# Performance work log

Hardware: AMD Instinct MI355X
Metric: run time of the kernel (lower is better)

The kernel has to match this reference:

```python
import jax, jax.numpy as jnp
import numpy as np

# --- constants matching DILConfig ---
N_DIFF = 1000      # num_diffusion_steps
STEPS = 4          # inference_steps
S_MAX = 4          # max_scales
BUDGET = 0.2       # entropy_budget
G0 = 2.0           # guidance_strength
ENT_LO = 0.1       # stability_threshold_low
ENT_HI = 0.5       # stability_threshold_high
B, L, C, H = 16, 1024, 128, 512


def setup_inputs() -> dict:
    key = jax.random.key(0)
    ks = jax.random.split(key, 6)
    y_obs = jax.random.normal(ks[0], (B, L, C), dtype=jnp.float32)
    mask = (jax.random.uniform(ks[1], (B, L, C)) > 0.5).astype(jnp.float32)
    z_init = jax.random.normal(ks[2], (B, L, C), dtype=jnp.float32)
    W1 = jax.random.normal(ks[3], (C, H), dtype=jnp.float32) / np.sqrt(C)
    b1 = jnp.zeros((H,), dtype=jnp.float32)
    W2 = jax.random.normal(ks[4], (H, C), dtype=jnp.float32) / np.sqrt(H)
    b2 = jnp.zeros((C,), dtype=jnp.float32)
    tw = jax.random.normal(ks[5], (H,), dtype=jnp.float32)
    return {"y_obs": y_obs, "mask": mask, "z_init": z_init,
            "W1": W1, "b1": b1, "W2": W2, "b2": b2, "tw": tw}


def _dil_forward(y_obs, mask, z_init, W1, b1, W2, b2, tw):
    # diffusion schedule (linear betas)
    betas = jnp.linspace(1e-4, 0.02, N_DIFF, dtype=jnp.float32)
    ac = jnp.cumprod(1.0 - betas)
    alpha = jnp.sqrt(ac)                     # sqrt_alphas_cumprod
    sigma = jnp.sqrt(1.0 - ac)               # sqrt_one_minus_alphas_cumprod
    lam = jnp.log(alpha) - jnp.log(sigma)    # log-SNR/2

    step = N_DIFF // STEPS
    ks = [N_DIFF - 1 - i * step for i in range(STEPS)]

    def score(z, k):
        # epsilon predictor: channel MLP with scalar time feature
        t_feat = jnp.float32(k) / N_DIFF
        h = jax.nn.gelu(jnp.einsum('blc,ch->blh', z, W1) + b1 + t_feat * tw)
        return jnp.einsum('blh,hc->blc', h, W2) + b2

    z = z_init
    for k in ks:  # fixed small unrolled loop over inference steps
        kp = max(k - step, 0)
        eps = score(z, k)                                   # [B,L,C]
        h_lam = lam[kp] - lam[k]
        base_a = alpha[kp] / alpha[k]
        base_b = sigma[kp] * (jnp.exp(h_lam) - 1.0)

        # entropy map: batch-mean |eps| per pixel
        ent_pix = jnp.mean(jnp.abs(eps), axis=0)            # [L,C]

        # self-guidance on observed entries
        obs_err = (z - y_obs) * mask
        guidance = -obs_err / (jnp.var(obs_err) + 1e-8)     # [B,L,C]

        z_new = z
        # coarse -> fine so finer-scale selected nodes overwrite coarser ones
        for s in range(S_MAX - 1, -1, -1):
            w = 2 ** s
            pooled = ent_pix.reshape(L // w, w, C // w, w).mean(axis=(1, 3))
            Knodes = max(1, int(BUDGET * pooled.size))
            _, idx = jax.lax.top_k(pooled.ravel(), Knodes)
            selg = jnp.zeros((pooled.size,), jnp.float32).at[idx].set(1.0)
            selg = selg.reshape(pooled.shape)
            sel = jnp.repeat(jnp.repeat(selg, w, axis=0), w, axis=1)     # [L,C]
            ent_up = jnp.repeat(jnp.repeat(pooled, w, axis=0), w, axis=1)

            # adaptive solver order from entropy stability thresholds
            order = (1.0 + (ent_up > ENT_LO).astype(jnp.float32)
                         + (ent_up > ENT_HI).astype(jnp.float32))
            corr = (1.0 + (order - 1.0) * 0.5 * h_lam
                        + (order - 1.0) * (order - 2.0) / 6.0 * h_lam ** 2)
            gs = G0 * ent_up / (ent_up + 1.0)               # adaptive guidance

            cand = base_a * z - base_b * (corr * eps) + gs * guidance
            z_new = jnp.where(sel[None, :, :] > 0, cand, z_new)
        z = z_new
    return z


def reference(y_obs, mask, z_init, W1, b1, W2, b2, tw):
    return _dil_forward(y_obs, mask, z_init, W1, b1, W2, b2, tw)
```

## Files before the change

kernel.cpp:

```cpp
#include <hip/hip_runtime.h>
#include <math.h>
#include <stdint.h>

#define L_DIM 1024
#define C_DIM 128
#define H_DIM 512
#define B_DIM 16
#define LC (L_DIM * C_DIM)
#define BLC (B_DIM * LC)

typedef __attribute__((ext_vector_type(8))) short short8;
typedef __attribute__((ext_vector_type(4))) float floatx4;

__device__ __forceinline__ unsigned fordbits(unsigned u) {
    return (u & 0x80000000u) ? ~u : (u | 0x80000000u);
}

__device__ __forceinline__ void split3(float x, unsigned& uh, unsigned& um,
                                       unsigned& ul) {
    uh = __float_as_uint(x);
    const float r1 = x - __uint_as_float(uh & 0xffff0000u);
    um = __float_as_uint(r1);
    const float r2 = r1 - __uint_as_float(um & 0xffff0000u);
    ul = __float_as_uint(r2);
}

__device__ __forceinline__ float gelu_fast(float x) {
    const float g = 0.7978845608028654f * (x + 0.044715f * x * x * x);
    const float e = __expf(2.0f * g);
    const float t = 1.0f - 2.0f / (e + 1.0f);
    return 0.5f * x * (1.0f + t);
}

__global__ __launch_bounds__(256) void wsplit_kernel(
    const float* __restrict__ W1, const float* __restrict__ W2,
    unsigned short* __restrict__ W1h, unsigned short* __restrict__ W1m,
    unsigned short* __restrict__ W1l, unsigned short* __restrict__ W2h,
    unsigned short* __restrict__ W2m, unsigned short* __restrict__ W2l,
    unsigned* __restrict__ zeroblk) {
    const int t = blockIdx.x * 256 + threadIdx.x;
    if (t < 16396) zeroblk[t] = 0u;
    unsigned uh, um, ul;
    if (t < 65536) {
        const int j = t & 7, lane = (t >> 3) & 63, nt = (t >> 9) & 31,
                  kt = (t >> 14) & 3;
        const int k = kt * 32 + (lane >> 4) * 8 + j;
        const int n = nt * 16 + (lane & 15);
        split3(W1[k * 512 + n], uh, um, ul);
        W1h[t] = (unsigned short)(uh >> 16);
        W1m[t] = (unsigned short)(um >> 16);
        W1l[t] = (unsigned short)(ul >> 16);
    } else {
        const int t2 = t - 65536;
        const int j = t2 & 7, lane = (t2 >> 3) & 63, nt = (t2 >> 9) & 7,
                  kt = (t2 >> 12) & 15;
        const int k = kt * 32 + (lane >> 4) * 8 + j;
        const int n = nt * 16 + (lane & 15);
        split3(W2[k * 128 + n], uh, um, ul);
        W2h[t2] = (unsigned short)(uh >> 16);
        W2m[t2] = (unsigned short)(um >> 16);
        W2l[t2] = (unsigned short)(ul >> 16);
    }
}

#define MFMA6(AH, AM, AL, BH, BM, BL, ACC)                                    \
    ACC = __builtin_amdgcn_mfma_f32_16x16x32_bf16(AL, BH, ACC, 0, 0, 0);      \
    ACC = __builtin_amdgcn_mfma_f32_16x16x32_bf16(AM, BM, ACC, 0, 0, 0);      \
    ACC = __builtin_amdgcn_mfma_f32_16x16x32_bf16(AH, BL, ACC, 0, 0, 0);      \
    ACC = __builtin_amdgcn_mfma_f32_16x16x32_bf16(AM, BH, ACC, 0, 0, 0);      \
    ACC = __builtin_amdgcn_mfma_f32_16x16x32_bf16(AH, BM, ACC, 0, 0, 0);      \
    ACC = __builtin_amdgcn_mfma_f32_16x16x32_bf16(AH, BH, ACC, 0, 0, 0);

__device__ __forceinline__ int swz(int row, int col) {
    return row * 128 + ((((col >> 3) ^ (row & 15))) << 3) + (col & 7);
}

template <int UPD>
__global__ __launch_bounds__(512, 2) void mlp_kernel(
    float* __restrict__ z, const float* __restrict__ zr,
    const float* __restrict__ y, const float* __restrict__ mk,
    const unsigned short* __restrict__ W1h, const unsigned short* __restrict__ W1m,
    const unsigned short* __restrict__ W1l, const unsigned short* __restrict__ W2h,
    const unsigned short* __restrict__ W2m, const unsigned short* __restrict__ W2l,
    const float* __restrict__ b1, const float* __restrict__ tw,
    const float* __restrict__ b2, float t_feat,
    float* __restrict__ eps_buf, float* __restrict__ ent,
    const float* __restrict__ cA, const float* __restrict__ cB,
    const float* __restrict__ cG, float* __restrict__ accum,
    float* __restrict__ p1, float* __restrict__ p2,
    unsigned* __restrict__ ghist) {
    __shared__ unsigned short zA[3][8192];
    __shared__ unsigned short hA[3][8192];
    __shared__ float entbuf[4][128];
    __shared__ float red1[8], red2[8];
    const int tid = threadIdx.x;
    const int w = tid >> 6, lane = tid & 63;
    const int quad = lane >> 4, m16 = lane & 15;
    const int l0 = blockIdx.x * 4;

    float s1 = 0.f, s2 = 0.f;
#pragma unroll
    for (int e = 0; e < 4; ++e) {
        const int f = (e * 512 + tid) * 4;
        const int r_ = f >> 7, cb = f & 127;
        const int b = r_ & 15, il = r_ >> 4, l = l0 + il;
        const size_t g = ((size_t)b * 1024 + l) * 128 + cb;
        float4 zv = *(const float4*)(zr + g);
        const float4 yv = *(const float4*)(y + g);
        const float4 mv = *(const float4*)(mk + g);
        if (UPD) {
            const float4 ev = *(const float4*)(eps_buf + g);
            const int pix = l * 128 + cb;
            const float4 a4 = *(const float4*)(cA + pix);
            const float4 b4 = *(const float4*)(cB + pix);
            const float4 g4 = *(const float4*)(cG + pix);
            zv.x = a4.x * zv.x - b4.x * ev.x - g4.x * ((zv.x - yv.x) * mv.x);
            zv.y = a4.y * zv.y - b4.y * ev.y - g4.y * ((zv.y - yv.y) * mv.y);
            zv.z = a4.z * zv.z - b4.z * ev.z - g4.z * ((zv.z - yv.z) * mv.z);
            zv.w = a4.w * zv.w - b4.w * ev.w - g4.w * ((zv.w - yv.w) * mv.w);
            *(float4*)(z + g) = zv;
        }
        float oe;
        oe = (zv.x - yv.x) * mv.x; s1 += oe; s2 += oe * oe;
        oe = (zv.y - yv.y) * mv.y; s1 += oe; s2 += oe * oe;
        oe = (zv.z - yv.z) * mv.z; s1 += oe; s2 += oe * oe;
        oe = (zv.w - yv.w) * mv.w; s1 += oe; s2 += oe * oe;

        const int base = swz(r_, cb);
        const float xs[4] = {zv.x, zv.y, zv.z, zv.w};
        ushort4 vh, vm, vl;
        unsigned uh, um, ul;
        split3(xs[0], uh, um, ul); vh.x = uh >> 16; vm.x = um >> 16; vl.x = ul >> 16;
        split3(xs[1], uh, um, ul); vh.y = uh >> 16; vm.y = um >> 16; vl.y = ul >> 16;
        split3(xs[2], uh, um, ul); vh.z = uh >> 16; vm.z = um >> 16; vl.z = ul >> 16;
        split3(xs[3], uh, um, ul); vh.w = uh >> 16; vm.w = um >> 16; vl.w = ul >> 16;
        *(ushort4*)(&zA[0][base]) = vh;
        *(ushort4*)(&zA[1][base]) = vm;
        *(ushort4*)(&zA[2][base]) = vl;
    }
#pragma unroll
    for (int off = 32; off; off >>= 1) {
        s1 += __shfl_down(s1, off);
        s2 += __shfl_down(s2, off);
    }
    if (lane == 0) { red1[w] = s1; red2[w] = s2; }
    __syncthreads();
    if (tid == 0) {
        float a1 = 0.f, a2 = 0.f;
#pragma unroll
        for (int i = 0; i < 8; ++i) { a1 += red1[i]; a2 += red2[i]; }
        atomicAdd(&accum[0], a1);
        atomicAdd(&accum[1], a2);
    }

    floatx4 acc1[16];
#pragma unroll
    for (int i = 0; i < 16; ++i) acc1[i] = (floatx4){0.f, 0.f, 0.f, 0.f};

    {
        short8 Ah[4], Am[4], Al[4];
        short8 bh, bm, bl;
        {
            const size_t off0 = ((size_t)w * 64 + lane) * 8;
            bh = *(const short8*)(W1h + off0);
            bm = *(const short8*)(W1m + off0);
            bl = *(const short8*)(W1l + off0);
        }
#pragma unroll
        for (int it = 0; it < 16; ++it) {
            const int kt = it >> 2, q = it & 3;
            if (q == 0) {
#pragma unroll
                for (int il = 0; il < 4; ++il) {
                    const int fb = swz(il * 16 + m16, kt * 32 + quad * 8);
                    Ah[il] = *(const short8*)(&zA[0][fb]);
                    Am[il] = *(const short8*)(&zA[1][fb]);
                    Al[il] = *(const short8*)(&zA[2][fb]);
                }
            }
            short8 nbh = bh, nbm = bm, nbl = bl;
            if (it < 15) {
                const int itn = it + 1;
                const size_t off =
                    ((size_t)((itn >> 2) * 32 + (itn & 3) * 8 + w) * 64 + lane) * 8;
                nbh = *(const short8*)(W1h + off);
                nbm = *(const short8*)(W1m + off);
                nbl = *(const short8*)(W1l + off);
            }
#pragma unroll
            for (int il = 0; il < 4; ++il) {
                floatx4 a = acc1[q * 4 + il];
                MFMA6(Ah[il], Am[il], Al[il], bh, bm, bl, a);
                acc1[q * 4 + il] = a;
            }
            bh = nbh; bm = nbm; bl = nbl;
        }
    }

    floatx4 acc2[4];
#pragma unroll
    for (int i = 0; i < 4; ++i) acc2[i] = (floatx4){0.f, 0.f, 0.f, 0.f};

    short8 ch, cm, cl;
    {
        const size_t off0 = ((size_t)w * 64 + lane) * 8;
        ch = *(const short8*)(W2h + off0);
        cm = *(const short8*)(W2m + off0);
        cl = *(const short8*)(W2l + off0);
    }
#pragma unroll
    for (int q = 0; q < 4; ++q) {
        {
            const int colg = q * 128 + w * 16 + m16;
            const float bb = b1[colg] + t_feat * tw[colg];
            const int kcol = w * 16 + m16;
#pragma unroll
            for (int il = 0; il < 4; ++il) {
#pragma unroll
                for (int r = 0; r < 4; ++r) {
                    const float x = gelu_fast(acc1[q * 4 + il][r] + bb);
                    unsigned uh, um, ul;
                    split3(x, uh, um, ul);
                    const int idx = swz(il * 16 + quad * 4 + r, kcol);
                    hA[0][idx] = (unsigned short)(uh >> 16);
                    hA[1][idx] = (unsigned short)(um >> 16);
                    hA[2][idx] = (unsigned short)(ul >> 16);
                }
            }
        }
        __syncthreads();

#pragma unroll
        for (int ktl = 0; ktl < 4; ++ktl) {
            const int jt = q * 4 + ktl;
            short8 nch = ch, ncm = cm, ncl = cl;
            if (jt < 15) {
                const size_t off = ((size_t)((jt + 1) * 8 + w) * 64 + lane) * 8;
                nch = *(const short8*)(W2h + off);
                ncm = *(const short8*)(W2m + off);
                ncl = *(const short8*)(W2l + off);
            }
            short8 Ah2[4], Am2[4], Al2[4];
#pragma unroll
            for (int il = 0; il < 4; ++il) {
                const int fb = swz(il * 16 + m16, ktl * 32 + quad * 8);
                Ah2[il] = *(const short8*)(&hA[0][fb]);
                Am2[il] = *(const short8*)(&hA[1][fb]);
                Al2[il] = *(const short8*)(&hA[2][fb]);
            }
#pragma unroll
            for (int il = 0; il < 4; ++il) {
                floatx4 a = acc2[il];
                MFMA6(Ah2[il], Am2[il], Al2[il], ch, cm, cl, a);
                acc2[il] = a;
            }
            ch = nch; cm = ncm; cl = ncl;
        }
        __syncthreads();
    }

    {
        const int col = w * 16 + m16;
        const float bb2 = b2[col];
#pragma unroll
        for (int il = 0; il < 4; ++il) {
            float pa = 0.f;
#pragma unroll
            for (int r = 0; r < 4; ++r) {
                const float e = acc2[il][r] + bb2;
                const int b = quad * 4 + r;
                eps_buf[((size_t)b * 1024 + l0 + il) * 128 + col] = e;
                pa += fabsf(e);
            }
            pa += __shfl_xor(pa, 16);
            pa += __shfl_xor(pa, 32);
            if (quad == 0) {
                const float ev = pa * (1.0f / 16.0f);
                ent[(l0 + il) * 128 + col] = ev;
                entbuf[il][col] = ev;
            }
        }
    }

    unsigned* lhist = (unsigned*)&hA[0][0];
    for (int i = tid; i < 8192; i += 512) lhist[i] = 0u;
    __syncthreads();
    if (tid < 512) {
        const float v = entbuf[tid >> 7][tid & 127];
        const unsigned b = fordbits(__float_as_uint(v)) >> 18;
        atomicAdd(&lhist[b >> 1], 1u << ((b & 1) << 4));
    }
    if (tid < 128) {
        const int ir = tid >> 6, c = tid & 63;
        float s = entbuf[2 * ir][2 * c];
        s += entbuf[2 * ir][2 * c + 1];
        s += entbuf[2 * ir + 1][2 * c];
        s += entbuf[2 * ir + 1][2 * c + 1];
        p1[(2 * (int)blockIdx.x + ir) * 64 + c] = s * 0.25f;
    }
    if (tid < 32) {
        const int c = tid;
        float s = 0.f;
#pragma unroll
        for (int ii = 0; ii < 4; ++ii) {
            s += entbuf[ii][4 * c];
            s += entbuf[ii][4 * c + 1];
            s += entbuf[ii][4 * c + 2];
            s += entbuf[ii][4 * c + 3];
        }
        p2[(int)blockIdx.x * 32 + c] = s * 0.0625f;
    }
    __syncthreads();
    for (int i = tid; i < 8192; i += 512) {
        const unsigned v = lhist[i];
        if (v & 0xFFFFu) atomicAdd(&ghist[2 * i], v & 0xFFFFu);
        if (v >> 16) atomicAdd(&ghist[2 * i + 1], v >> 16);
    }
}


#define CAND_CAP 16384

template <int NPT4, int N, unsigned K>
__device__ __forceinline__ void small_select_vals(
    const float4* xv, unsigned* __restrict__ gout, const int t,
    const int w8, unsigned* __restrict__ histcand,
    unsigned* __restrict__ part, unsigned (*hrep)[512],
    unsigned* sh_b, unsigned* sh_krem, unsigned* sh_cnt, unsigned* sh_d,
    unsigned* sh_k2) {
    unsigned u[NPT4 * 4];
#pragma unroll
    for (int i = 0; i < NPT4; ++i) {
        u[4 * i + 0] = fordbits(__float_as_uint(xv[i].x));
        u[4 * i + 1] = fordbits(__float_as_uint(xv[i].y));
        u[4 * i + 2] = fordbits(__float_as_uint(xv[i].z));
        u[4 * i + 3] = fordbits(__float_as_uint(xv[i].w));
    }
    if (t == 0) { *sh_b = 0u; *sh_krem = 1u; *sh_cnt = 0u; *sh_d = 0u; *sh_k2 = 1u; }
    for (int i = t; i < 16384; i += 1024) histcand[i] = 0u;
    __syncthreads();
#pragma unroll
    for (int j = 0; j < NPT4 * 4; ++j) atomicAdd(&histcand[u[j] >> 18], 1u);
    __syncthreads();
    {
        unsigned s = 0;
#pragma unroll
        for (int j = 0; j < 16; ++j) s += histcand[t * 16 + j];
        part[t] = s;
    }
    __syncthreads();
    for (int off = 1; off < 1024; off <<= 1) {
        const unsigned v = (t + off < 1024) ? part[t + off] : 0u;
        __syncthreads();
        part[t] += v;
        __syncthreads();
    }
    {
        const unsigned suf = part[t];
        const unsigned sufn = (t < 1023) ? part[t + 1] : 0u;
        if (suf >= K && sufn < K) {
            unsigned run = sufn;
            for (int b = 15; b >= 0; --b) {
                const unsigned hb = histcand[t * 16 + b];
                run += hb;
                if (run >= K) {
                    *sh_b = (unsigned)(t * 16 + b);
                    *sh_krem = K - (run - hb);
                    break;
                }
            }
        }
    }
    __syncthreads();
    const unsigned b14 = *sh_b;
    unsigned krem = *sh_krem;
    __syncthreads();
#pragma unroll
    for (int j = 0; j < NPT4 * 4; ++j)
        if ((u[j] >> 18) == b14) {
            const unsigned p = atomicAdd(sh_cnt, 1u);
            if (p < CAND_CAP) histcand[p] = u[j];
        }
    __syncthreads();
    const unsigned cnt = *sh_cnt;
    const bool inlds = (cnt <= CAND_CAP);
    for (int i = t; i < 4096; i += 1024) ((unsigned*)hrep)[i] = 0u;
    __syncthreads();
    if (inlds) {
        for (unsigned i = t; i < cnt; i += 1024)
            atomicAdd(&hrep[w8][(histcand[i] >> 9) & 511u], 1u);
    } else {
#pragma unroll
        for (int j = 0; j < NPT4 * 4; ++j)
            if ((u[j] >> 18) == b14)
                atomicAdd(&hrep[w8][(u[j] >> 9) & 511u], 1u);
    }
    __syncthreads();
    if (t < 512) {
        unsigned s = 0;
#pragma unroll
        for (int r = 0; r < 8; ++r) s += hrep[r][t];
        part[t] = s;
    }
    __syncthreads();
    for (int off = 1; off < 512; off <<= 1) {
        unsigned v = 0u;
        if (t < 512) v = (t + off < 512) ? part[t + off] : 0u;
        __syncthreads();
        if (t < 512) part[t] += v;
        __syncthreads();
    }
    if (t < 512) {
        const unsigned suf = part[t];
        const unsigned sufn = (t < 511) ? part[t + 1] : 0u;
        if (suf >= krem && sufn < krem) { *sh_d = (unsigned)t; *sh_k2 = krem - sufn; }
    }
    __syncthreads();
    const unsigned dA = *sh_d;
    krem = *sh_k2;
    __syncthreads();
    for (int i = t; i < 4096; i += 1024) ((unsigned*)hrep)[i] = 0u;
    __syncthreads();
    if (inlds) {
        for (unsigned i = t; i < cnt; i += 1024) {
            const unsigned c = histcand[i];
            if (((c >> 9) & 511u) == dA) atomicAdd(&hrep[w8][c & 511u], 1u);
        }
    } else {
#pragma unroll
        for (int j = 0; j < NPT4 * 4; ++j)
            if ((u[j] >> 18) == b14 && ((u[j] >> 9) & 511u) == dA)
                atomicAdd(&hrep[w8][u[j] & 511u], 1u);
    }
    __syncthreads();
    if (t < 512) {
        unsigned s = 0;
#pragma unroll
        for (int r = 0; r < 8; ++r) s += hrep[r][t];
        part[t] = s;
    }
    __syncthreads();
    for (int off = 1; off < 512; off <<= 1) {
        unsigned v = 0u;
        if (t < 512) v = (t + off < 512) ? part[t + off] : 0u;
        __syncthreads();
        if (t < 512) part[t] += v;
        __syncthreads();
    }
    if (t < 512) {
        const unsigned suf = part[t];
        const unsigned sufn = (t < 511) ? part[t + 1] : 0u;
        if (suf >= krem && sufn < krem)
            gout[0] = (b14 << 18) | (dA << 9) | (unsigned)t;
    }
}

__global__ __launch_bounds__(1024, 1) void thresh_kernel(
    const float* __restrict__ ent, const float* __restrict__ p1,
    const float* __restrict__ p2, float* __restrict__ p3,
    const unsigned* __restrict__ ghist, unsigned* __restrict__ gprefix) {
    const int scale = blockIdx.x, t = threadIdx.x;
    __shared__ unsigned histcand[16384];
    __shared__ unsigned part[1024];
    __shared__ unsigned hrep[8][512];
    __shared__ unsigned sh_b, sh_krem, sh_cnt, sh_d, sh_k2;
    const int w8 = (t >> 6) & 7;

    if (scale == 1) {
        float4 xv[8];
#pragma unroll
        for (int i = 0; i < 8; ++i) xv[i] = ((const float4*)p1)[t + i * 1024];
        small_select_vals<8, 32768, 6553u>(xv, &gprefix[1], t, w8, histcand,
                                           part, hrep, &sh_b, &sh_krem,
                                           &sh_cnt, &sh_d, &sh_k2);
        return;
    }
    if (scale == 2) {
        float4 xv[2];
#pragma unroll
        for (int i = 0; i < 2; ++i) xv[i] = ((const float4*)p2)[t + i * 1024];
        small_select_vals<2, 8192, 1638u>(xv, &gprefix[2], t, w8, histcand,
                                          part, hrep, &sh_b, &sh_krem,
                                          &sh_cnt, &sh_d, &sh_k2);
        return;
    }
    if (scale == 3) {
        float4 xv[1];
        if (t < 512) {
            float sv[4];
#pragma unroll
            for (int jdx = 0; jdx < 4; ++jdx) {
                const int e = t * 4 + jdx;
                const int r = e >> 4, c = e & 15;
                float s = 0.f;
#pragma unroll
                for (int ii = 0; ii < 8; ++ii) {
                    const float4 ea =
                        *(const float4*)(ent + (((r * 8 + ii) << 7) + c * 8));
                    const float4 eb =
                        *(const float4*)(ent + (((r * 8 + ii) << 7) + c * 8 + 4));
                    s += ea.x; s += ea.y; s += ea.z; s += ea.w;
                    s += eb.x; s += eb.y; s += eb.z; s += eb.w;
                }
                sv[jdx] = s * (1.0f / 64.0f);
            }
            xv[0] = (float4){sv[0], sv[1], sv[2], sv[3]};
            *(float4*)(p3 + t * 4) = xv[0];
        } else {
            xv[0] = (float4){-1e30f, -1e30f, -1e30f, -1e30f};
        }
        small_select_vals<1, 2048, 409u>(xv, &gprefix[3], t, w8, histcand,
                                         part, hrep, &sh_b, &sh_krem,
                                         &sh_cnt, &sh_d, &sh_k2);
        return;
    }

    const unsigned K = 26214u;
    if (t == 0) { sh_b = 0u; sh_krem = 1u; sh_cnt = 0u; sh_d = 0u; sh_k2 = 1u; }

    {
        unsigned s = 0;
        const uint4* h4 = (const uint4*)(ghist + t * 16);
#pragma unroll
        for (int j = 0; j < 4; ++j) {
            const uint4 x = h4[j];
            s += x.x + x.y + x.z + x.w;
        }
        part[t] = s;
    }
    __syncthreads();
    for (int off = 1; off < 1024; off <<= 1) {
        const unsigned v = (t + off < 1024) ? part[t + off] : 0u;
        __syncthreads();
        part[t] += v;
        __syncthreads();
    }
    {
        const unsigned suf = part[t];
        const unsigned sufn = (t < 1023) ? part[t + 1] : 0u;
        if (suf >= K && sufn < K) {
            unsigned run = sufn;
            for (int b = 15; b >= 0; --b) {
                const unsigned hb = ghist[t * 16 + b];
                run += hb;
                if (run >= K) {
                    sh_b = (unsigned)(t * 16 + b);
                    sh_krem = K - (run - hb);
                    break;
                }
            }
        }
    }
    __syncthreads();
    const unsigned b14 = sh_b;
    unsigned krem = sh_krem;

    for (int base = 0; base < 32768; base += 8192) {
        float4 w4[8];
#pragma unroll
        for (int i = 0; i < 8; ++i)
            w4[i] = ((const float4*)ent)[base + i * 1024 + t];
#pragma unroll
        for (int i = 0; i < 8; ++i) {
            const float xs[4] = {w4[i].x, w4[i].y, w4[i].z, w4[i].w};
#pragma unroll
            for (int j = 0; j < 4; ++j) {
                const unsigned uu = fordbits(__float_as_uint(xs[j]));
                if ((uu >> 18) == b14) {
                    const unsigned p = atomicAdd(&sh_cnt, 1u);
                    if (p < CAND_CAP) histcand[p] = uu;
                }
            }
        }
    }
    __syncthreads();
    const unsigned cnt = sh_cnt;
    const bool inlds = (cnt <= CAND_CAP);

    for (int i = t; i < 4096; i += 1024) ((unsigned*)hrep)[i] = 0u;
    __syncthreads();
    if (inlds) {
        for (unsigned i = t; i < cnt; i += 1024)
            atomicAdd(&hrep[w8][(histcand[i] >> 9) & 511u], 1u);
    } else {
        for (int base = 0; base < 32768; base += 8192) {
            float4 w4[8];
#pragma unroll
            for (int i = 0; i < 8; ++i)
                w4[i] = ((const float4*)ent)[base + i * 1024 + t];
#pragma unroll
            for (int i = 0; i < 8; ++i) {
                const float xs[4] = {w4[i].x, w4[i].y, w4[i].z, w4[i].w};
#pragma unroll
                for (int j = 0; j < 4; ++j) {
                    const unsigned uu = fordbits(__float_as_uint(xs[j]));
                    if ((uu >> 18) == b14)
                        atomicAdd(&hrep[w8][(uu >> 9) & 511u], 1u);
                }
            }
        }
    }
    __syncthreads();
    if (t < 512) {
        unsigned s = 0;
#pragma unroll
        for (int r = 0; r < 8; ++r) s += hrep[r][t];
        part[t] = s;
    }
    __syncthreads();
    for (int off = 1; off < 512; off <<= 1) {
        unsigned v = 0u;
        if (t < 512) v = (t + off < 512) ? part[t + off] : 0u;
        __syncthreads();
        if (t < 512) part[t] += v;
        __syncthreads();
    }
    if (t < 512) {
        const unsigned suf = part[t];
        const unsigned sufn = (t < 511) ? part[t + 1] : 0u;
        if (suf >= krem && sufn < krem) { sh_d = (unsigned)t; sh_k2 = krem - sufn; }
    }
    __syncthreads();
    const unsigned dA = sh_d;
    krem = sh_k2;
    __syncthreads();

    for (int i = t; i < 4096; i += 1024) ((unsigned*)hrep)[i] = 0u;
    __syncthreads();
    if (inlds) {
        for (unsigned i = t; i < cnt; i += 1024) {
            const unsigned c = histcand[i];
            if (((c >> 9) & 511u) == dA) atomicAdd(&hrep[w8][c & 511u], 1u);
        }
    } else {
        for (int base = 0; base < 32768; base += 8192) {
            float4 w4[8];
#pragma unroll
            for (int i = 0; i < 8; ++i)
                w4[i] = ((const float4*)ent)[base + i * 1024 + t];
#pragma unroll
            for (int i = 0; i < 8; ++i) {
                const float xs[4] = {w4[i].x, w4[i].y, w4[i].z, w4[i].w};
#pragma unroll
                for (int j = 0; j < 4; ++j) {
                    const unsigned uu = fordbits(__float_as_uint(xs[j]));
                    if ((uu >> 18) == b14 && ((uu >> 9) & 511u) == dA)
                        atomicAdd(&hrep[w8][uu & 511u], 1u);
                }
            }
        }
    }
    __syncthreads();
    if (t < 512) {
        unsigned s = 0;
#pragma unroll
        for (int r = 0; r < 8; ++r) s += hrep[r][t];
        part[t] = s;
    }
    __syncthreads();
    for (int off = 1; off < 512; off <<= 1) {
        unsigned v = 0u;
        if (t < 512) v = (t + off < 512) ? part[t + off] : 0u;
        __syncthreads();
        if (t < 512) part[t] += v;
        __syncthreads();
    }
    if (t < 512) {
        const unsigned suf = part[t];
        const unsigned sufn = (t < 511) ? part[t + 1] : 0u;
        if (suf >= krem && sufn < krem)
            gprefix[0] = (b14 << 18) | (dA << 9) | (unsigned)t;
    }
}

__global__ __launch_bounds__(256) void coeff_kernel(
    const float* __restrict__ ent, const float* __restrict__ p1,
    const float* __restrict__ p2, const float* __restrict__ p3,
    const unsigned* __restrict__ gprefix, const float* __restrict__ accum_si,
    float* __restrict__ cA, float* __restrict__ cB, float* __restrict__ cG,
    unsigned* __restrict__ ghist, float base_a, float base_b, float h_lam) {
    const int i = blockIdx.x * 256 + threadIdx.x;
    if (i < 16384) ghist[i] = 0u;

    const unsigned t0 = gprefix[0], t1 = gprefix[1], t2 = gprefix[2],
                   t3 = gprefix[3];
    const float mean = accum_si[0] * (1.0f / (float)BLC);
    const float var = accum_si[1] * (1.0f / (float)BLC) - mean * mean;
    const float vinv = 1.0f / (var + 1e-8f);

    const int l = i >> 7, c = i & 127;
    float ent_v = 0.f;
    bool sel = false;
    const float v0 = ent[i];
    if (fordbits(__float_as_uint(v0)) >= t0) { ent_v = v0; sel = true; }
    else {
        const float v1 = p1[((l >> 1) << 6) + (c >> 1)];
        if (fordbits(__float_as_uint(v1)) >= t1) { ent_v = v1; sel = true; }
        else {
            const float v2 = p2[((l >> 2) << 5) + (c >> 2)];
            if (fordbits(__float_as_uint(v2)) >= t2) { ent_v = v2; sel = true; }
            else {
                const float v3 = p3[((l >> 3) << 4) + (c >> 3)];
                if (fordbits(__float_as_uint(v3)) >= t3) { ent_v = v3; sel = true; }
            }
        }
    }
    if (sel) {
        float corr;
        if (ent_v > 0.5f)
            corr = 1.0f + h_lam + h_lam * h_lam * (1.0f / 3.0f);
        else if (ent_v > 0.1f)
            corr = 1.0f + 0.5f * h_lam;
        else
            corr = 1.0f;
        cA[i] = base_a;
        cB[i] = base_b * corr;
        cG[i] = (2.0f * ent_v / (ent_v + 1.0f)) * vinv;
    } else {
        cA[i] = 1.0f;
        cB[i] = 0.f;
        cG[i] = 0.f;
    }
}

__global__ __launch_bounds__(256) void update_kernel(
    float* __restrict__ z, const float* __restrict__ y,
    const float* __restrict__ mk, const float* __restrict__ eps,
    const float* __restrict__ cA, const float* __restrict__ cB,
    const float* __restrict__ cG) {
    const int idx = blockIdx.x * 256 + threadIdx.x;
    const int p = idx & (LC - 1);
    const float zi = z[idx];
    z[idx] = cA[p] * zi - cB[p] * eps[idx] - cG[p] * ((zi - y[idx]) * mk[idx]);
}

extern "C" void kernel_launch(void* const* d_in, const int* in_sizes, int n_in,
                              void* d_out, int out_size, void* d_ws,
                              size_t ws_size, hipStream_t stream) {
    const float* y_obs = (const float*)d_in[0];
    const float* mask = (const float*)d_in[1];
    const float* z_init = (const float*)d_in[2];
    const float* W1 = (const float*)d_in[3];
    const float* b1 = (const float*)d_in[4];
    const float* W2 = (const float*)d_in[5];
    const float* b2 = (const float*)d_in[6];
    const float* tw = (const float*)d_in[7];
    float* z = (float*)d_out;
    float* ws = (float*)d_ws;

    float* eps = ws;
    float* ent = ws + 2097152;
    float* p1 = ws + 2228224;
    float* p2 = ws + 2260992;
    float* p3 = ws + 2269184;
    float* cA = ws + 2271232;
    float* cB = ws + 2402304;
    float* cG = ws + 2533376;
    float* accum = ws + 2664448;
    unsigned* gprefix = (unsigned*)(ws + 2664456);
    unsigned* ghist = (unsigned*)(ws + 2664460);
    unsigned short* W1h = (unsigned short*)(ws + 2680844);
    unsigned short* W1m = (unsigned short*)(ws + 2713612);
    unsigned short* W1l = (unsigned short*)(ws + 2746380);
    unsigned short* W2h = (unsigned short*)(ws + 2779148);
    unsigned short* W2m = (unsigned short*)(ws + 2811916);
    unsigned short* W2l = (unsigned short*)(ws + 2844684);

    float alpha_[1000], sigma_[1000], lam_[1000];
    {
        float ac = 1.0f;
        for (int i = 0; i < 1000; ++i) {
            const float beta = 1e-4f + (0.02f - 1e-4f) * ((float)i / 999.0f);
            ac = ac * (1.0f - beta);
            alpha_[i] = sqrtf(ac);
            sigma_[i] = sqrtf(1.0f - ac);
            lam_[i] = logf(alpha_[i]) - logf(sigma_[i]);
        }
    }
    float tf[4], hl[4], ba[4], bb[4];
    for (int si = 0; si < 4; ++si) {
        const int k = 999 - si * 250;
        const int kp = (k - 250 > 0) ? (k - 250) : 0;
        tf[si] = (float)k / 1000.0f;
        hl[si] = lam_[kp] - lam_[k];
        ba[si] = alpha_[kp] / alpha_[k];
        bb[si] = sigma_[kp] * (expf(hl[si]) - 1.0f);
    }

    wsplit_kernel<<<512, 256, 0, stream>>>(W1, W2, W1h, W1m, W1l, W2h, W2m,
                                           W2l, (unsigned*)accum);

    for (int si = 0; si < 4; ++si) {
        const float* zrd = (si <= 1) ? z_init : z;
        if (si == 0) {
            mlp_kernel<0><<<256, 512, 0, stream>>>(
                z, zrd, y_obs, mask, W1h, W1m, W1l, W2h, W2m, W2l, b1, tw, b2,
                tf[0], eps, ent, cA, cB, cG, accum, p1, p2, ghist);
        } else {
            mlp_kernel<1><<<256, 512, 0, stream>>>(
                z, zrd, y_obs, mask, W1h, W1m, W1l, W2h, W2m, W2l, b1, tw, b2,
                tf[si], eps, ent, cA, cB, cG, accum + 2 * si, p1, p2, ghist);
        }
        thresh_kernel<<<4, 1024, 0, stream>>>(ent, p1, p2, p3, ghist, gprefix);
        coeff_kernel<<<512, 256, 0, stream>>>(ent, p1, p2, p3, gprefix,
                                              accum + 2 * si, cA, cB, cG,
                                              ghist, ba[si], bb[si], hl[si]);
    }
    update_kernel<<<8192, 256, 0, stream>>>(z, y_obs, mask, eps, cA, cB, cG);
}
```

Baseline: 370.5 us.

## Replace barrier-heavy LDS suffix scans with wave-shuffle scans and drop weight prefetch

```diff
diff --git a/kernel.cpp b/kernel.cpp
--- a/kernel.cpp
+++ b/kernel.cpp
@@ -157,43 +157,28 @@
 #pragma unroll
     for (int i = 0; i < 16; ++i) acc1[i] = (floatx4){0.f, 0.f, 0.f, 0.f};
 
-    {
+#pragma unroll
+    for (int kt = 0; kt < 4; ++kt) {
         short8 Ah[4], Am[4], Al[4];
-        short8 bh, bm, bl;
-        {
-            const size_t off0 = ((size_t)w * 64 + lane) * 8;
-            bh = *(const short8*)(W1h + off0);
-            bm = *(const short8*)(W1m + off0);
-            bl = *(const short8*)(W1l + off0);
-        }
-#pragma unroll
-        for (int it = 0; it < 16; ++it) {
-            const int kt = it >> 2, q = it & 3;
-            if (q == 0) {
-#pragma unroll
-                for (int il = 0; il < 4; ++il) {
-                    const int fb = swz(il * 16 + m16, kt * 32 + quad * 8);
-                    Ah[il] = *(const short8*)(&zA[0][fb]);
-                    Am[il] = *(const short8*)(&zA[1][fb]);
-                    Al[il] = *(const short8*)(&zA[2][fb]);
-                }
-            }
-            short8 nbh = bh, nbm = bm, nbl = bl;
-            if (it < 15) {
-                const int itn = it + 1;
-                const size_t off =
-                    ((size_t)((itn >> 2) * 32 + (itn & 3) * 8 + w) * 64 + lane) * 8;
-                nbh = *(const short8*)(W1h + off);
-                nbm = *(const short8*)(W1m + off);
-                nbl = *(const short8*)(W1l + off);
-            }
+#pragma unroll
+        for (int il = 0; il < 4; ++il) {
+            const int fb = swz(il * 16 + m16, kt * 32 + quad * 8);
+            Ah[il] = *(const short8*)(&zA[0][fb]);
+            Am[il] = *(const short8*)(&zA[1][fb]);
+            Al[il] = *(const short8*)(&zA[2][fb]);
+        }
+#pragma unroll
+        for (int q = 0; q < 4; ++q) {
+            const size_t off = ((size_t)(kt * 32 + q * 8 + w) * 64 + lane) * 8;
+            const short8 bh = *(const short8*)(W1h + off);
+            const short8 bm = *(const short8*)(W1m + off);
+            const short8 bl = *(const short8*)(W1l + off);
 #pragma unroll
             for (int il = 0; il < 4; ++il) {
                 floatx4 a = acc1[q * 4 + il];
                 MFMA6(Ah[il], Am[il], Al[il], bh, bm, bl, a);
                 acc1[q * 4 + il] = a;
             }
-            bh = nbh; bm = nbm; bl = nbl;
         }
     }
 
@@ -201,13 +186,6 @@
 #pragma unroll
     for (int i = 0; i < 4; ++i) acc2[i] = (floatx4){0.f, 0.f, 0.f, 0.f};
 
-    short8 ch, cm, cl;
-    {
-        const size_t off0 = ((size_t)w * 64 + lane) * 8;
-        ch = *(const short8*)(W2h + off0);
-        cm = *(const short8*)(W2m + off0);
-        cl = *(const short8*)(W2l + off0);
-    }
 #pragma unroll
     for (int q = 0; q < 4; ++q) {
         {
@@ -232,14 +210,6 @@
 
 #pragma unroll
         for (int ktl = 0; ktl < 4; ++ktl) {
-            const int jt = q * 4 + ktl;
-            short8 nch = ch, ncm = cm, ncl = cl;
-            if (jt < 15) {
-                const size_t off = ((size_t)((jt + 1) * 8 + w) * 64 + lane) * 8;
-                nch = *(const short8*)(W2h + off);
-                ncm = *(const short8*)(W2m + off);
-                ncl = *(const short8*)(W2l + off);
-            }
             short8 Ah2[4], Am2[4], Al2[4];
 #pragma unroll
             for (int il = 0; il < 4; ++il) {
@@ -248,13 +218,17 @@
                 Am2[il] = *(const short8*)(&hA[1][fb]);
                 Al2[il] = *(const short8*)(&hA[2][fb]);
             }
+            const size_t off =
+                ((size_t)((q * 4 + ktl) * 8 + w) * 64 + lane) * 8;
+            const short8 bh = *(const short8*)(W2h + off);
+            const short8 bm = *(const short8*)(W2m + off);
+            const short8 bl = *(const short8*)(W2l + off);
 #pragma unroll
             for (int il = 0; il < 4; ++il) {
                 floatx4 a = acc2[il];
-                MFMA6(Ah2[il], Am2[il], Al2[il], ch, cm, cl, a);
+                MFMA6(Ah2[il], Am2[il], Al2[il], bh, bm, bl, a);
                 acc2[il] = a;
             }
-            ch = nch; cm = ncm; cl = ncl;
         }
         __syncthreads();
     }
@@ -319,6 +293,27 @@
 }
 
 
+__device__ __forceinline__ void suffix_scan_block(unsigned* __restrict__ part,
+                                                  unsigned* __restrict__ wtot,
+                                                  const int n, const int t) {
+    const int lane = t & 63, w = t >> 6;
+    const int nw = n >> 6;
+    unsigned s = (t < n) ? part[t] : 0u;
+#pragma unroll
+    for (int off = 1; off < 64; off <<= 1) {
+        const unsigned v = __shfl_down(s, off);
+        if (lane + off < 64) s += v;
+    }
+    if (t < n && lane == 0) wtot[w] = s;
+    __syncthreads();
+    if (t < n) {
+        unsigned o = 0;
+        for (int j = w + 1; j < nw; ++j) o += wtot[j];
+        part[t] = s + o;
+    }
+    __syncthreads();
+}
+
 #define CAND_CAP 16384
 
 template <int NPT4, int N, unsigned K>
@@ -326,6 +321,7 @@
     const float4* xv, unsigned* __restrict__ gout, const int t,
     const int w8, unsigned* __restrict__ histcand,
     unsigned* __restrict__ part, unsigned (*hrep)[512],
+    unsigned* __restrict__ wtot,
     unsigned* sh_b, unsigned* sh_krem, unsigned* sh_cnt, unsigned* sh_d,
     unsigned* sh_k2) {
     unsigned u[NPT4 * 4];
@@ -348,13 +344,7 @@
         for (int j = 0; j < 16; ++j) s += histcand[t * 16 + j];
         part[t] = s;
     }
-    __syncthreads();
-    for (int off = 1; off < 1024; off <<= 1) {
-        const unsigned v = (t + off < 1024) ? part[t + off] : 0u;
-        __syncthreads();
-        part[t] += v;
-        __syncthreads();
-    }
+    suffix_scan_block(part, wtot, 1024, t);
     {
         const unsigned suf = part[t];
         const unsigned sufn = (t < 1023) ? part[t + 1] : 0u;
@@ -403,13 +393,7 @@
         part[t] = s;
     }
     __syncthreads();
-    for (int off = 1; off < 512; off <<= 1) {
-        unsigned v = 0u;
-        if (t < 512) v = (t + off < 512) ? part[t + off] : 0u;
-        __syncthreads();
-        if (t < 512) part[t] += v;
-        __syncthreads();
-    }
+    suffix_scan_block(part, wtot, 512, t);
     if (t < 512) {
         const unsigned suf = part[t];
         const unsigned sufn = (t < 511) ? part[t + 1] : 0u;
@@ -440,13 +424,7 @@
         part[t] = s;
     }
     __syncthreads();
-    for (int off = 1; off < 512; off <<= 1) {
-        unsigned v = 0u;
-        if (t < 512) v = (t + off < 512) ? part[t + off] : 0u;
-        __syncthreads();
-        if (t < 512) part[t] += v;
-        __syncthreads();
-    }
+    suffix_scan_block(part, wtot, 512, t);
     if (t < 512) {
         const unsigned suf = part[t];
         const unsigned sufn = (t < 511) ? part[t + 1] : 0u;
@@ -463,6 +441,7 @@
     __shared__ unsigned histcand[16384];
     __shared__ unsigned part[1024];
     __shared__ unsigned hrep[8][512];
+    __shared__ unsigned wtot[16];
     __shared__ unsigned sh_b, sh_krem, sh_cnt, sh_d, sh_k2;
     const int w8 = (t >> 6) & 7;
 
@@ -471,7 +450,7 @@
 #pragma unroll
         for (int i = 0; i < 8; ++i) xv[i] = ((const float4*)p1)[t + i * 1024];
         small_select_vals<8, 32768, 6553u>(xv, &gprefix[1], t, w8, histcand,
-                                           part, hrep, &sh_b, &sh_krem,
+                                           part, hrep, wtot, &sh_b, &sh_krem,
                                            &sh_cnt, &sh_d, &sh_k2);
         return;
     }
@@ -480,7 +459,7 @@
 #pragma unroll
         for (int i = 0; i < 2; ++i) xv[i] = ((const float4*)p2)[t + i * 1024];
         small_select_vals<2, 8192, 1638u>(xv, &gprefix[2], t, w8, histcand,
-                                          part, hrep, &sh_b, &sh_krem,
+                                          part, hrep, wtot, &sh_b, &sh_krem,
                                           &sh_cnt, &sh_d, &sh_k2);
         return;
     }
@@ -510,7 +489,7 @@
             xv[0] = (float4){-1e30f, -1e30f, -1e30f, -1e30f};
         }
         small_select_vals<1, 2048, 409u>(xv, &gprefix[3], t, w8, histcand,
-                                         part, hrep, &sh_b, &sh_krem,
+                                         part, hrep, wtot, &sh_b, &sh_krem,
                                          &sh_cnt, &sh_d, &sh_k2);
         return;
     }
@@ -529,12 +508,7 @@
         part[t] = s;
     }
     __syncthreads();
-    for (int off = 1; off < 1024; off <<= 1) {
-        const unsigned v = (t + off < 1024) ? part[t + off] : 0u;
-        __syncthreads();
-        part[t] += v;
-        __syncthreads();
-    }
+    suffix_scan_block(part, wtot, 1024, t);
     {
         const unsigned suf = part[t];
         const unsigned sufn = (t < 1023) ? part[t + 1] : 0u;
@@ -608,13 +582,7 @@
         part[t] = s;
     }
     __syncthreads();
-    for (int off = 1; off < 512; off <<= 1) {
-        unsigned v = 0u;
-        if (t < 512) v = (t + off < 512) ? part[t + off] : 0u;
-        __syncthreads();
-        if (t < 512) part[t] += v;
-        __syncthreads();
-    }
+    suffix_scan_block(part, wtot, 512, t);
     if (t < 512) {
         const unsigned suf = part[t];
         const unsigned sufn = (t < 511) ? part[t + 1] : 0u;
@@ -658,13 +626,7 @@
         part[t] = s;
     }
     __syncthreads();
-    for (int off = 1; off < 512; off <<= 1) {
-        unsigned v = 0u;
-        if (t < 512) v = (t + off < 512) ? part[t + off] : 0u;
-        __syncthreads();
-        if (t < 512) part[t] += v;
-        __syncthreads();
-    }
+    suffix_scan_block(part, wtot, 512, t);
     if (t < 512) {
         const unsigned suf = part[t];
         const unsigned sufn = (t < 511) ? part[t + 1] : 0u;
```

New measurement: 374.4 us. About the same (+1.1%).
